# Performance work log

Measured on AMD Instinct MI355X. Metric: run time of the kernel, lower is better.

## Reference

```python
import jax, jax.numpy as jnp
import numpy as np

EPS_DENOM = 1e-7   # epsilon added to sigmoid-sum denominator in the torch code
EPS_NORM = 1e-5    # torch InstanceNorm1d default eps


def _fcnn(x, W1, b1, W2, b2):
    # FCNN: Linear -> ReLU -> Linear
    return jax.nn.relu(x @ W1 + b1) @ W2 + b2


def setup_inputs() -> dict:
    key = jax.random.key(0)
    N, E, D, H = 100000, 1600000, 32, 128  # nodes, edges, feature dim (c_in1=c_out2), hidden (c_out1)
    ks = jax.random.split(key, 11)
    node_features = jax.random.normal(ks[0], (N, D), jnp.float32)
    edge_features = jax.random.normal(ks[1], (E, D), jnp.float32)
    edge_index = jax.random.randint(ks[2], (2, E), 0, N, dtype=jnp.int64)
    sD = 1.0 / np.sqrt(D)
    sH = 1.0 / np.sqrt(H)
    # FCNN_one params
    W1a = jax.random.normal(ks[3], (D, H), jnp.float32) * sD
    b1a = jax.random.normal(ks[4], (H,), jnp.float32) * sD
    W2a = jax.random.normal(ks[5], (H, D), jnp.float32) * sH
    b2a = jax.random.normal(ks[6], (D,), jnp.float32) * sH
    # FCNN_two params
    W1b = jax.random.normal(ks[7], (D, H), jnp.float32) * sD
    b1b = jax.random.normal(ks[8], (H,), jnp.float32) * sD
    W2b = jax.random.normal(ks[9], (H, D), jnp.float32) * sH
    b2b = jax.random.normal(ks[10], (D,), jnp.float32) * sH
    return dict(node_features=node_features, edge_features=edge_features,
                W1a=W1a, b1a=b1a, W2a=W2a, b2a=b2a,
                W1b=W1b, b1b=b1b, W2b=W2b, b2b=b2b,
                edge_index=edge_index)


def reference(node_features, edge_features, W1a, b1a, W2a, b2a,
              W1b, b1b, W2b, b2b, edge_index):
    x = node_features                      # [N, D]
    N = x.shape[0]
    h1 = _fcnn(x, W1a, b1a, W2a, b2a)      # FCNN_one(x_i) for all nodes
    h2 = _fcnn(x, W1b, b1b, W2b, b2b)      # FCNN_two(x_j) for all nodes

    s = jax.nn.sigmoid(edge_features)      # [E, D]
    # node i gathers edges where it is src OR dst (both directions)
    seg = jnp.concatenate([edge_index[0], edge_index[1]])  # [2E] center node
    nbr = jnp.concatenate([edge_index[1], edge_index[0]])  # [2E] neighbor node
    s2 = jnp.concatenate([s, s], axis=0)                   # [2E, D]

    denom = EPS_DENOM + jax.ops.segment_sum(s2, seg, num_segments=N)  # [N, D]
    msg = (s2 / denom[seg]) * h2[nbr]                                 # [2E, D]
    agg = jax.ops.segment_sum(msg, seg, num_segments=N)               # [N, D]

    h = h1 + agg
    # InstanceNorm1d over the feature dim (no affine, biased variance); dropout is identity (eval)
    mu = jnp.mean(h, axis=-1, keepdims=True)
    var = jnp.var(h, axis=-1, keepdims=True)
    hn = (h - mu) * jax.lax.rsqrt(var + EPS_NORM)
    return x + jax.nn.relu(hn)
```

## Files before the change

### kernel.cpp

```cpp
#include <hip/hip_runtime.h>

#define EPS_DENOM 1e-7f
#define EPS_NORM  1e-5f

static constexpr int D  = 32;
static constexpr int H  = 128;
static constexpr int BK = 128;
static constexpr int CHUNK = 3072;
static constexpr int CAPMAX = 6144;

typedef _Float16 f16x8 __attribute__((ext_vector_type(8)));
typedef float    f32x4 __attribute__((ext_vector_type(4)));

__global__ __launch_bounds__(256) void fcnn_mfma_kernel(
    const float* __restrict__ x,
    const float* __restrict__ W1a, const float* __restrict__ b1a,
    const float* __restrict__ W2a, const float* __restrict__ b2a,
    const float* __restrict__ W1b, const float* __restrict__ b1b,
    const float* __restrict__ W2b, const float* __restrict__ b2b,
    float* __restrict__ h1, _Float16* __restrict__ h2h, int N)
{
    __shared__ _Float16 lds[30208];
    _Float16* xk = lds;

    const int tid = threadIdx.x;
    const int nb0 = blockIdx.x * 64;

    #pragma unroll
    for (int t = 0; t < 8; ++t) {
        int f = t * 256 + tid;
        int node = f >> 5, off = f & 31;
        int gn = nb0 + node;
        float v = (gn < N) ? x[(size_t)gn * 32 + off] : 0.0f;
        xk[node * 40 + off] = (_Float16)v;
    }
    for (int fc = 0; fc < 2; ++fc) {
        const float* W1 = fc ? W1b : W1a;
        const float* W2 = fc ? W2b : W2a;
        _Float16* w1t = lds + 2560 + fc * 5120;
        _Float16* w2t = lds + 12800 + fc * 4352;
        #pragma unroll
        for (int t = 0; t < 16; ++t) {
            int f = t * 256 + tid;
            w1t[(f & 127) * 40 + (f >> 7)] = (_Float16)W1[f];
        }
        #pragma unroll
        for (int t = 0; t < 16; ++t) {
            int f = t * 256 + tid;
            w2t[(f & 31) * 136 + (f >> 5)] = (_Float16)W2[f];
        }
    }
    __syncthreads();

    const int wid  = tid >> 6;
    const int lane = tid & 63;
    const int m    = lane & 15;
    const int g    = lane >> 4;
    _Float16* t1 = lds + 21504 + wid * 2176;

    f16x8 ax = *(const f16x8*)(xk + (wid * 16 + m) * 40 + g * 8);

    for (int fc = 0; fc < 2; ++fc) {
        const float* b1v = fc ? b1b : b1a;
        const float* b2v = fc ? b2b : b2a;
        const _Float16* w1t = lds + 2560 + fc * 5120;
        const _Float16* w2t = lds + 12800 + fc * 4352;

        for (int hb = 0; hb < 8; ++hb) {
            f16x8 bw = *(const f16x8*)(w1t + (hb * 16 + m) * 40 + g * 8);
            f32x4 c = {0.f, 0.f, 0.f, 0.f};
            c = __builtin_amdgcn_mfma_f32_16x16x32_f16(ax, bw, c, 0, 0, 0);
            float bias = b1v[hb * 16 + m];
            #pragma unroll
            for (int r = 0; r < 4; ++r) {
                float tv = fmaxf(c[r] + bias, 0.0f);
                t1[(g * 4 + r) * 136 + hb * 16 + m] = (_Float16)tv;
            }
        }

        for (int dt = 0; dt < 2; ++dt) {
            f32x4 c2 = {0.f, 0.f, 0.f, 0.f};
            #pragma unroll
            for (int kc = 0; kc < 4; ++kc) {
                f16x8 a2  = *(const f16x8*)(t1 + m * 136 + kc * 32 + g * 8);
                f16x8 b2w = *(const f16x8*)(w2t + (dt * 16 + m) * 136 + kc * 32 + g * 8);
                c2 = __builtin_amdgcn_mfma_f32_16x16x32_f16(a2, b2w, c2, 0, 0, 0);
            }
            float bias = b2v[dt * 16 + m];
            #pragma unroll
            for (int r = 0; r < 4; ++r) {
                int gn = nb0 + wid * 16 + g * 4 + r;
                if (gn < N) {
                    float val = c2[r] + bias;
                    if (fc == 0) h1[(size_t)gn * 32 + dt * 16 + m] = val;
                    else         h2h[(size_t)gn * 32 + dt * 16 + m] = (_Float16)val;
                }
            }
        }
        __syncthreads();
    }
}

__global__ __launch_bounds__(256) void sprep_kernel(
    const float* __restrict__ ef, _Float16* __restrict__ sgh, int n4)
{
    int i = blockIdx.x * blockDim.x + threadIdx.x;
    if (i >= n4) return;
    float4 v = ((const float4*)ef)[i];
    _Float16 r[4];
    r[0] = (_Float16)(1.0f / (1.0f + __expf(-v.x)));
    r[1] = (_Float16)(1.0f / (1.0f + __expf(-v.y)));
    r[2] = (_Float16)(1.0f / (1.0f + __expf(-v.z)));
    r[3] = (_Float16)(1.0f / (1.0f + __expf(-v.w)));
    ((uint2*)sgh)[i] = *(const uint2*)r;
}

__global__ __launch_bounds__(256) void bin1_kernel(
    const int* __restrict__ ei, int* __restrict__ gcursor,
    uint2* __restrict__ gadj, int E, int CAP)
{
    __shared__ uint2 recs[2 * CHUNK];
    __shared__ int cnt[1024];
    __shared__ int offs[1024];
    __shared__ int gbase[1024];
    __shared__ int partial[256];

    const int tid  = threadIdx.x;
    const int base = blockIdx.x * CHUNK;
    const int ne   = min(CHUNK, E - base);

    #pragma unroll
    for (int i = 0; i < 4; ++i) cnt[tid * 4 + i] = 0;
    __syncthreads();

    int av[CHUNK / 256], bv[CHUNK / 256];
    #pragma unroll
    for (int j = 0; j < CHUNK / 256; ++j) {
        int r = j * 256 + tid;
        if (r < ne) {
            int e = base + r;
            av[j] = ei[e]; bv[j] = ei[E + e];
            atomicAdd(&cnt[av[j] >> 7], 1);
            atomicAdd(&cnt[bv[j] >> 7], 1);
        } else av[j] = -1;
    }
    __syncthreads();

    int c0 = cnt[tid*4], c1 = cnt[tid*4+1], c2 = cnt[tid*4+2], c3 = cnt[tid*4+3];
    int psum = c0 + c1 + c2 + c3;
    partial[tid] = psum;
    __syncthreads();
    for (int off = 1; off < 256; off <<= 1) {
        int t = (tid >= off) ? partial[tid - off] : 0;
        __syncthreads();
        partial[tid] += t;
        __syncthreads();
    }
    int ex = partial[tid] - psum;
    offs[tid*4]   = ex;
    offs[tid*4+1] = ex + c0;
    offs[tid*4+2] = ex + c0 + c1;
    offs[tid*4+3] = ex + c0 + c1 + c2;
    cnt[tid*4]    = ex;
    cnt[tid*4+1]  = ex + c0;
    cnt[tid*4+2]  = ex + c0 + c1;
    cnt[tid*4+3]  = ex + c0 + c1 + c2;
    __syncthreads();

    #pragma unroll
    for (int j = 0; j < CHUNK / 256; ++j) {
        if (av[j] >= 0) {
            int e = base + j * 256 + tid;
            int a = av[j], b = bv[j];
            int pa = atomicAdd(&cnt[a >> 7], 1);
            recs[pa] = make_uint2(((unsigned)(a & 127) << 21) | (unsigned)e,
                                  ((unsigned)(a >> 7) << 17) | (unsigned)b);
            int pb = atomicAdd(&cnt[b >> 7], 1);
            recs[pb] = make_uint2(((unsigned)(b & 127) << 21) | (unsigned)e,
                                  ((unsigned)(b >> 7) << 17) | (unsigned)a);
        }
    }
    __syncthreads();

    #pragma unroll
    for (int i = 0; i < 4; ++i) {
        int bidx = tid * 4 + i;
        int c = cnt[bidx] - offs[bidx];
        if (c > 0) gbase[bidx] = atomicAdd(&gcursor[bidx], c);
    }
    __syncthreads();

    int total = 2 * ne;
    for (int i = tid; i < total; i += 256) {
        uint2 r = recs[i];
        int bidx = r.y >> 17;
        int dest = gbase[bidx] + (i - offs[bidx]);
        if (dest < CAP)
            gadj[(size_t)bidx * CAP + dest] = r;
    }
}

__global__ __launch_bounds__(256) void bin2_kernel(
    const int* __restrict__ gcursor, uint2* __restrict__ gadj,
    int* __restrict__ gstart, int* __restrict__ gdeg,
    int N, int CAP)
{
    __shared__ uint2 recs[CAPMAX];
    __shared__ int cnt[BK];
    __shared__ int sc[BK];
    __shared__ int lcur[BK];

    const int tid = threadIdx.x;
    const int bk  = blockIdx.x;
    const int count = min(gcursor[bk], CAP);
    uint2* seg = gadj + (size_t)bk * CAP;

    if (tid < BK) cnt[tid] = 0;
    for (int i = tid; i < count; i += 256) recs[i] = seg[i];
    __syncthreads();

    for (int i = tid; i < count; i += 256)
        atomicAdd(&cnt[(recs[i].x >> 21) & 127], 1);
    __syncthreads();

    int v = (tid < BK) ? cnt[tid] : 0;
    if (tid < BK) sc[tid] = v;
    __syncthreads();
    for (int off = 1; off < BK; off <<= 1) {
        int t = (tid < BK && tid >= off) ? sc[tid - off] : 0;
        __syncthreads();
        if (tid < BK) sc[tid] += t;
        __syncthreads();
    }
    if (tid < BK) {
        int excl = sc[tid] - v;
        lcur[tid] = excl;
        int gn = bk * BK + tid;
        if (gn < N) {
            gstart[gn] = bk * CAP + excl;
            gdeg[gn]   = v;
        }
    }
    __syncthreads();

    for (int i = tid; i < count; i += 256) {
        uint2 r = recs[i];
        int l = (r.x >> 21) & 127;
        int pos = atomicAdd(&lcur[l], 1);
        seg[pos] = make_uint2(r.x & 0x1FFFFFu, r.y & 0x1FFFFu);
    }
}

template <bool USE_SG>
__global__ __launch_bounds__(256) void gather_kernel(
    const float* __restrict__ x,  const _Float16* __restrict__ sgh,
    const float* __restrict__ ef, const float* __restrict__ h1,
    const _Float16* __restrict__ h2h,
    const int* __restrict__ gstart, const int* __restrict__ gdeg,
    const uint2* __restrict__ adj2,
    float* __restrict__ out, int N)
{
    int t = blockIdx.x * blockDim.x + threadIdx.x;
    int n = t >> 5;
    int d = t & 31;
    if (n >= N) return;

    int start = gstart[n];
    int end   = start + gdeg[n];

    float s_sum = 0.0f, sh_sum = 0.0f;
    int k = start;
    for (; k + 4 <= end; k += 4) {
        uint2 r0 = adj2[k+0], r1 = adj2[k+1], r2 = adj2[k+2], r3 = adj2[k+3];
        float s0, s1, s2, s3;
        if (USE_SG) {
            s0 = (float)sgh[(size_t)r0.x * 32 + d];
            s1 = (float)sgh[(size_t)r1.x * 32 + d];
            s2 = (float)sgh[(size_t)r2.x * 32 + d];
            s3 = (float)sgh[(size_t)r3.x * 32 + d];
        } else {
            s0 = 1.0f / (1.0f + __expf(-ef[(size_t)r0.x * 32 + d]));
            s1 = 1.0f / (1.0f + __expf(-ef[(size_t)r1.x * 32 + d]));
            s2 = 1.0f / (1.0f + __expf(-ef[(size_t)r2.x * 32 + d]));
            s3 = 1.0f / (1.0f + __expf(-ef[(size_t)r3.x * 32 + d]));
        }
        float h0 = (float)h2h[(size_t)r0.y * 32 + d];
        float h1v = (float)h2h[(size_t)r1.y * 32 + d];
        float h2v = (float)h2h[(size_t)r2.y * 32 + d];
        float h3 = (float)h2h[(size_t)r3.y * 32 + d];
        s_sum += (s0 + s1) + (s2 + s3);
        sh_sum = fmaf(s0, h0, sh_sum);
        sh_sum = fmaf(s1, h1v, sh_sum);
        sh_sum = fmaf(s2, h2v, sh_sum);
        sh_sum = fmaf(s3, h3, sh_sum);
    }
    for (; k < end; ++k) {
        uint2 r = adj2[k];
        float s;
        if (USE_SG) s = (float)sgh[(size_t)r.x * 32 + d];
        else        s = 1.0f / (1.0f + __expf(-ef[(size_t)r.x * 32 + d]));
        float hh = (float)h2h[(size_t)r.y * 32 + d];
        s_sum += s;
        sh_sum = fmaf(s, hh, sh_sum);
    }

    size_t idx = (size_t)n * 32 + d;
    float h = h1[idx] + sh_sum / (EPS_DENOM + s_sum);

    float sum = h, sq = h * h;
    #pragma unroll
    for (int off = 16; off > 0; off >>= 1) {
        sum += __shfl_xor(sum, off, 32);
        sq  += __shfl_xor(sq,  off, 32);
    }
    float mu  = sum * (1.0f / 32.0f);
    float var = fmaxf(sq * (1.0f / 32.0f) - mu * mu, 0.0f);
    float hn  = (h - mu) * rsqrtf(var + EPS_NORM);

    out[idx] = x[idx] + fmaxf(hn, 0.0f);
}

extern "C" void kernel_launch(void* const* d_in, const int* in_sizes, int n_in,
                              void* d_out, int out_size, void* d_ws, size_t ws_size,
                              hipStream_t stream)
{
    const float* x   = (const float*)d_in[0];
    const float* ef  = (const float*)d_in[1];
    const float* W1a = (const float*)d_in[2];
    const float* b1a = (const float*)d_in[3];
    const float* W2a = (const float*)d_in[4];
    const float* b2a = (const float*)d_in[5];
    const float* W1b = (const float*)d_in[6];
    const float* b1b = (const float*)d_in[7];
    const float* W2b = (const float*)d_in[8];
    const float* b2b = (const float*)d_in[9];
    const int*   ei  = (const int*)d_in[10];
    float* out = (float*)d_out;

    const int N  = in_sizes[0] / D;
    const int E  = in_sizes[1] / D;
    const int NB = (N + BK - 1) / BK;
    int CAP = (2 * E) / NB;
    CAP = CAP + CAP / 2;
    CAP = (CAP + 255) & ~255;
    if (CAP > CAPMAX) CAP = CAPMAX;

    char* p = (char*)d_ws;
    float*    h1      = (float*)p;    p += (size_t)N * 32 * 4;
    _Float16* h2h     = (_Float16*)p; p += (size_t)N * 32 * 2;
    int*      gcursor = (int*)p;      p += 1024 * 4;
    int*      gstart  = (int*)p;      p += (size_t)N * 4;
    int*      gdeg    = (int*)p;      p += (size_t)N * 4;
    uint2*    gadj    = (uint2*)p;    p += (size_t)NB * CAP * 8;
    _Float16* sgh     = (_Float16*)p;
    const bool use_sg = ((size_t)(p - (char*)d_ws) + (size_t)E * 64) <= ws_size;

    hipMemsetAsync(gcursor, 0, 1024 * 4, stream);

    fcnn_mfma_kernel<<<(N + 63) / 64, 256, 0, stream>>>(
        x, W1a, b1a, W2a, b2a, W1b, b1b, W2b, b2b, h1, h2h, N);

    if (use_sg) {
        int n4 = E * 8;
        sprep_kernel<<<(n4 + 255) / 256, 256, 0, stream>>>(ef, sgh, n4);
    }

    bin1_kernel<<<(E + CHUNK - 1) / CHUNK, 256, 0, stream>>>(ei, gcursor, gadj, E, CAP);
    bin2_kernel<<<NB, 256, 0, stream>>>(gcursor, gadj, gstart, gdeg, N, CAP);

    int gthreads = N * 32;
    if (use_sg)
        gather_kernel<true><<<(gthreads + 255) / 256, 256, 0, stream>>>(
            x, sgh, ef, h1, h2h, gstart, gdeg, gadj, out, N);
    else
        gather_kernel<false><<<(gthreads + 255) / 256, 256, 0, stream>>>(
            x, sgh, ef, h1, h2h, gstart, gdeg, gadj, out, N);
}
```

Before: 558.4 us.

## Fuse sigmoid into binning and scatter 8-bit quantized payloads per adjacency slot

Removes the separate sigmoid-precompute kernel. The binning kernel now computes the sigmoid of each edge's features, quantizes them to 8 bits in LDS, and writes a 32-byte payload alongside each adjacency record into per-bucket storage. The gather kernel then reads these payloads from bucket-local memory rather than from scattered fp16 rows. This cuts the bytes per edge gather and improves locality. In exchange the sigmoid has only 8-bit precision (error up to about 0.002), which may hurt accuracy, and the binning chunk shrinks to fit the extra LDS, which adds more blocks and more global atomics.

```diff
diff --git a/kernel.cpp b/kernel.cpp
--- a/kernel.cpp
+++ b/kernel.cpp
@@ -6,7 +6,7 @@
 static constexpr int D  = 32;
 static constexpr int H  = 128;
 static constexpr int BK = 128;
-static constexpr int CHUNK = 3072;
+static constexpr int CHUNK = 1024;
 static constexpr int CAPMAX = 6144;
 
 typedef _Float16 f16x8 __attribute__((ext_vector_type(8)));
@@ -101,25 +101,13 @@
     }
 }
 
-__global__ __launch_bounds__(256) void sprep_kernel(
-    const float* __restrict__ ef, _Float16* __restrict__ sgh, int n4)
-{
-    int i = blockIdx.x * blockDim.x + threadIdx.x;
-    if (i >= n4) return;
-    float4 v = ((const float4*)ef)[i];
-    _Float16 r[4];
-    r[0] = (_Float16)(1.0f / (1.0f + __expf(-v.x)));
-    r[1] = (_Float16)(1.0f / (1.0f + __expf(-v.y)));
-    r[2] = (_Float16)(1.0f / (1.0f + __expf(-v.z)));
-    r[3] = (_Float16)(1.0f / (1.0f + __expf(-v.w)));
-    ((uint2*)sgh)[i] = *(const uint2*)r;
-}
-
 __global__ __launch_bounds__(256) void bin1_kernel(
-    const int* __restrict__ ei, int* __restrict__ gcursor,
-    uint2* __restrict__ gadj, int E, int CAP)
+    const int* __restrict__ ei, const float* __restrict__ ef,
+    int* __restrict__ gcursor, uint2* __restrict__ gadj,
+    unsigned char* __restrict__ pay, int E, int CAP, int paymode)
 {
     __shared__ uint2 recs[2 * CHUNK];
+    __shared__ uint4 srows4[CHUNK * 2];
     __shared__ int cnt[1024];
     __shared__ int offs[1024];
     __shared__ int gbase[1024];
@@ -143,6 +131,25 @@
             atomicAdd(&cnt[av[j] >> 7], 1);
             atomicAdd(&cnt[bv[j] >> 7], 1);
         } else av[j] = -1;
+    }
+
+    if (paymode) {
+        const float4* efc = (const float4*)(ef + (size_t)base * 32);
+        uchar4* sc4 = (uchar4*)srows4;
+        const int nf4 = ne * 8;
+        #pragma unroll
+        for (int j = 0; j < CHUNK * 8 / 256; ++j) {
+            int fidx = j * 256 + tid;
+            if (fidx < nf4) {
+                float4 v = efc[fidx];
+                uchar4 q;
+                q.x = (unsigned char)(255.0f / (1.0f + __expf(-v.x)) + 0.5f);
+                q.y = (unsigned char)(255.0f / (1.0f + __expf(-v.y)) + 0.5f);
+                q.z = (unsigned char)(255.0f / (1.0f + __expf(-v.z)) + 0.5f);
+                q.w = (unsigned char)(255.0f / (1.0f + __expf(-v.w)) + 0.5f);
+                sc4[fidx] = q;
+            }
+        }
     }
     __syncthreads();
 
@@ -190,20 +197,30 @@
     }
     __syncthreads();
 
+    const unsigned char* srows = (const unsigned char*)srows4;
     int total = 2 * ne;
     for (int i = tid; i < total; i += 256) {
         uint2 r = recs[i];
         int bidx = r.y >> 17;
         int dest = gbase[bidx] + (i - offs[bidx]);
-        if (dest < CAP)
-            gadj[(size_t)bidx * CAP + dest] = r;
+        if (dest < CAP) {
+            size_t slot = (size_t)bidx * CAP + dest;
+            gadj[slot] = r;
+            if (paymode) {
+                int le = (int)(r.x & 0x1FFFFFu) - base;
+                const uint4* sr = (const uint4*)(srows + le * 32);
+                uint4 s0 = sr[0], s1 = sr[1];
+                uint4* pd = (uint4*)(pay + slot * 32);
+                pd[0] = s0; pd[1] = s1;
+            }
+        }
     }
 }
 
 __global__ __launch_bounds__(256) void bin2_kernel(
     const int* __restrict__ gcursor, uint2* __restrict__ gadj,
     int* __restrict__ gstart, int* __restrict__ gdeg,
-    int N, int CAP)
+    int N, int CAP, int paymode)
 {
     __shared__ uint2 recs[CAPMAX];
     __shared__ int cnt[BK];
@@ -247,18 +264,19 @@
         uint2 r = recs[i];
         int l = (r.x >> 21) & 127;
         int pos = atomicAdd(&lcur[l], 1);
-        seg[pos] = make_uint2(r.x & 0x1FFFFFu, r.y & 0x1FFFFu);
-    }
-}
-
-template <bool USE_SG>
+        unsigned xv = paymode ? (unsigned)i : (r.x & 0x1FFFFFu);
+        seg[pos] = make_uint2(xv, r.y & 0x1FFFFu);
+    }
+}
+
+template <int MODE>
 __global__ __launch_bounds__(256) void gather_kernel(
-    const float* __restrict__ x,  const _Float16* __restrict__ sgh,
-    const float* __restrict__ ef, const float* __restrict__ h1,
-    const _Float16* __restrict__ h2h,
+    const float* __restrict__ x,  const float* __restrict__ ef,
+    const unsigned char* __restrict__ pay,
+    const float* __restrict__ h1, const _Float16* __restrict__ h2h,
     const int* __restrict__ gstart, const int* __restrict__ gdeg,
     const uint2* __restrict__ adj2,
-    float* __restrict__ out, int N)
+    float* __restrict__ out, int N, int CAP)
 {
     int t = blockIdx.x * blockDim.x + threadIdx.x;
     int n = t >> 5;
@@ -267,17 +285,18 @@
 
     int start = gstart[n];
     int end   = start + gdeg[n];
+    const unsigned char* payb = pay + (size_t)(n >> 7) * CAP * 32 + d;
 
     float s_sum = 0.0f, sh_sum = 0.0f;
     int k = start;
     for (; k + 4 <= end; k += 4) {
         uint2 r0 = adj2[k+0], r1 = adj2[k+1], r2 = adj2[k+2], r3 = adj2[k+3];
         float s0, s1, s2, s3;
-        if (USE_SG) {
-            s0 = (float)sgh[(size_t)r0.x * 32 + d];
-            s1 = (float)sgh[(size_t)r1.x * 32 + d];
-            s2 = (float)sgh[(size_t)r2.x * 32 + d];
-            s3 = (float)sgh[(size_t)r3.x * 32 + d];
+        if (MODE) {
+            s0 = (float)payb[(size_t)r0.x * 32] * (1.0f / 255.0f);
+            s1 = (float)payb[(size_t)r1.x * 32] * (1.0f / 255.0f);
+            s2 = (float)payb[(size_t)r2.x * 32] * (1.0f / 255.0f);
+            s3 = (float)payb[(size_t)r3.x * 32] * (1.0f / 255.0f);
         } else {
             s0 = 1.0f / (1.0f + __expf(-ef[(size_t)r0.x * 32 + d]));
             s1 = 1.0f / (1.0f + __expf(-ef[(size_t)r1.x * 32 + d]));
@@ -297,8 +316,8 @@
     for (; k < end; ++k) {
         uint2 r = adj2[k];
         float s;
-        if (USE_SG) s = (float)sgh[(size_t)r.x * 32 + d];
-        else        s = 1.0f / (1.0f + __expf(-ef[(size_t)r.x * 32 + d]));
+        if (MODE) s = (float)payb[(size_t)r.x * 32] * (1.0f / 255.0f);
+        else      s = 1.0f / (1.0f + __expf(-ef[(size_t)r.x * 32 + d]));
         float hh = (float)h2h[(size_t)r.y * 32 + d];
         s_sum += s;
         sh_sum = fmaf(s, hh, sh_sum);
@@ -351,28 +370,28 @@
     int*      gcursor = (int*)p;      p += 1024 * 4;
     int*      gstart  = (int*)p;      p += (size_t)N * 4;
     int*      gdeg    = (int*)p;      p += (size_t)N * 4;
+    p = (char*)(((uintptr_t)p + 31) & ~(uintptr_t)31);
     uint2*    gadj    = (uint2*)p;    p += (size_t)NB * CAP * 8;
-    _Float16* sgh     = (_Float16*)p;
-    const bool use_sg = ((size_t)(p - (char*)d_ws) + (size_t)E * 64) <= ws_size;
+    p = (char*)(((uintptr_t)p + 31) & ~(uintptr_t)31);
+    unsigned char* pay = (unsigned char*)p;
+    const bool use_pay =
+        ((size_t)(p - (char*)d_ws) + (size_t)NB * CAP * 32) <= ws_size;
+    const int paymode = use_pay ? 1 : 0;
 
     hipMemsetAsync(gcursor, 0, 1024 * 4, stream);
 
     fcnn_mfma_kernel<<<(N + 63) / 64, 256, 0, stream>>>(
         x, W1a, b1a, W2a, b2a, W1b, b1b, W2b, b2b, h1, h2h, N);
 
-    if (use_sg) {
-        int n4 = E * 8;
-        sprep_kernel<<<(n4 + 255) / 256, 256, 0, stream>>>(ef, sgh, n4);
-    }
-
-    bin1_kernel<<<(E + CHUNK - 1) / CHUNK, 256, 0, stream>>>(ei, gcursor, gadj, E, CAP);
-    bin2_kernel<<<NB, 256, 0, stream>>>(gcursor, gadj, gstart, gdeg, N, CAP);
+    bin1_kernel<<<(E + CHUNK - 1) / CHUNK, 256, 0, stream>>>(
+        ei, ef, gcursor, gadj, pay, E, CAP, paymode);
+    bin2_kernel<<<NB, 256, 0, stream>>>(gcursor, gadj, gstart, gdeg, N, CAP, paymode);
 
     int gthreads = N * 32;
-    if (use_sg)
-        gather_kernel<true><<<(gthreads + 255) / 256, 256, 0, stream>>>(
-            x, sgh, ef, h1, h2h, gstart, gdeg, gadj, out, N);
+    if (use_pay)
+        gather_kernel<1><<<(gthreads + 255) / 256, 256, 0, stream>>>(
+            x, ef, pay, h1, h2h, gstart, gdeg, gadj, out, N, CAP);
     else
-        gather_kernel<false><<<(gthreads + 255) / 256, 256, 0, stream>>>(
-            x, sgh, ef, h1, h2h, gstart, gdeg, gadj, out, N);
-}
+        gather_kernel<0><<<(gthreads + 255) / 256, 256, 0, stream>>>(
+            x, ef, pay, h1, h2h, gstart, gdeg, gadj, out, N, CAP);
+}
```

Result: slower. 652.3 us (+16.8%).

## Fuse local sort and gather into per-bucket LDS-atomic aggregation kernel

Applied to the files above, without the earlier changes.

Replaces the second binning pass (per-node counting sort within each bucket) and the per-node gather kernel with one kernel per 128-node bucket. That kernel accumulates sigmoid and sigmoid*h2 sums into shared-memory arrays with atomics, then applies instance norm and writes the output. It also drops the fp16 sigmoid precompute pass and computes the sigmoid from the fp32 edge features inline. This removes a kernel launch, the gstart/gdeg arrays and a global rewrite of the adjacency, at the cost of LDS atomic contention and reading fp32 edge features instead of fp16.

```diff
diff --git a/kernel.cpp b/kernel.cpp
--- a/kernel.cpp
+++ b/kernel.cpp
@@ -7,7 +7,6 @@
 static constexpr int H  = 128;
 static constexpr int BK = 128;
 static constexpr int CHUNK = 3072;
-static constexpr int CAPMAX = 6144;
 
 typedef _Float16 f16x8 __attribute__((ext_vector_type(8)));
 typedef float    f32x4 __attribute__((ext_vector_type(4)));
@@ -101,20 +100,6 @@
     }
 }
 
-__global__ __launch_bounds__(256) void sprep_kernel(
-    const float* __restrict__ ef, _Float16* __restrict__ sgh, int n4)
-{
-    int i = blockIdx.x * blockDim.x + threadIdx.x;
-    if (i >= n4) return;
-    float4 v = ((const float4*)ef)[i];
-    _Float16 r[4];
-    r[0] = (_Float16)(1.0f / (1.0f + __expf(-v.x)));
-    r[1] = (_Float16)(1.0f / (1.0f + __expf(-v.y)));
-    r[2] = (_Float16)(1.0f / (1.0f + __expf(-v.z)));
-    r[3] = (_Float16)(1.0f / (1.0f + __expf(-v.w)));
-    ((uint2*)sgh)[i] = *(const uint2*)r;
-}
-
 __global__ __launch_bounds__(256) void bin1_kernel(
     const int* __restrict__ ei, int* __restrict__ gcursor,
     uint2* __restrict__ gadj, int E, int CAP)
@@ -200,124 +185,79 @@
     }
 }
 
-__global__ __launch_bounds__(256) void bin2_kernel(
-    const int* __restrict__ gcursor, uint2* __restrict__ gadj,
-    int* __restrict__ gstart, int* __restrict__ gdeg,
-    int N, int CAP)
+__global__ __launch_bounds__(512) void agg_kernel(
+    const int* __restrict__ gcursor, const uint2* __restrict__ gadj,
+    const float* __restrict__ ef, const float* __restrict__ x,
+    const float* __restrict__ h1, const _Float16* __restrict__ h2h,
+    float* __restrict__ out, int N, int CAP)
 {
-    __shared__ uint2 recs[CAPMAX];
-    __shared__ int cnt[BK];
-    __shared__ int sc[BK];
-    __shared__ int lcur[BK];
+    __shared__ float acc_s [BK * 32];
+    __shared__ float acc_sh[BK * 32];
 
     const int tid = threadIdx.x;
     const int bk  = blockIdx.x;
     const int count = min(gcursor[bk], CAP);
-    uint2* seg = gadj + (size_t)bk * CAP;
-
-    if (tid < BK) cnt[tid] = 0;
-    for (int i = tid; i < count; i += 256) recs[i] = seg[i];
-    __syncthreads();
-
-    for (int i = tid; i < count; i += 256)
-        atomicAdd(&cnt[(recs[i].x >> 21) & 127], 1);
-    __syncthreads();
-
-    int v = (tid < BK) ? cnt[tid] : 0;
-    if (tid < BK) sc[tid] = v;
-    __syncthreads();
-    for (int off = 1; off < BK; off <<= 1) {
-        int t = (tid < BK && tid >= off) ? sc[tid - off] : 0;
-        __syncthreads();
-        if (tid < BK) sc[tid] += t;
-        __syncthreads();
-    }
-    if (tid < BK) {
-        int excl = sc[tid] - v;
-        lcur[tid] = excl;
-        int gn = bk * BK + tid;
-        if (gn < N) {
-            gstart[gn] = bk * CAP + excl;
-            gdeg[gn]   = v;
-        }
-    }
-    __syncthreads();
-
-    for (int i = tid; i < count; i += 256) {
-        uint2 r = recs[i];
+    const uint2* seg = gadj + (size_t)bk * CAP;
+
+    for (int i = tid; i < BK * 32; i += 512) {
+        acc_s[i]  = 0.0f;
+        acc_sh[i] = 0.0f;
+    }
+    __syncthreads();
+
+    const int g = tid >> 5;
+    const int d = tid & 31;
+
+    int k = g;
+    for (; k + 16 < count; k += 32) {
+        uint2 r0 = seg[k];
+        uint2 r1 = seg[k + 16];
+        int e0 = r0.x & 0x1FFFFF, e1 = r1.x & 0x1FFFFF;
+        float v0 = ef[(size_t)e0 * 32 + d];
+        float v1 = ef[(size_t)e1 * 32 + d];
+        float hv0 = (float)h2h[(size_t)(r0.y & 0x1FFFF) * 32 + d];
+        float hv1 = (float)h2h[(size_t)(r1.y & 0x1FFFF) * 32 + d];
+        float s0 = 1.0f / (1.0f + __expf(-v0));
+        float s1 = 1.0f / (1.0f + __expf(-v1));
+        int l0 = (r0.x >> 21) & 127;
+        int l1 = (r1.x >> 21) & 127;
+        atomicAdd(&acc_s [l0 * 32 + d], s0);
+        atomicAdd(&acc_sh[l0 * 32 + d], s0 * hv0);
+        atomicAdd(&acc_s [l1 * 32 + d], s1);
+        atomicAdd(&acc_sh[l1 * 32 + d], s1 * hv1);
+    }
+    if (k < count) {
+        uint2 r = seg[k];
+        int e = r.x & 0x1FFFFF;
+        float v = ef[(size_t)e * 32 + d];
+        float hv = (float)h2h[(size_t)(r.y & 0x1FFFF) * 32 + d];
+        float s = 1.0f / (1.0f + __expf(-v));
         int l = (r.x >> 21) & 127;
-        int pos = atomicAdd(&lcur[l], 1);
-        seg[pos] = make_uint2(r.x & 0x1FFFFFu, r.y & 0x1FFFFu);
-    }
-}
-
-template <bool USE_SG>
-__global__ __launch_bounds__(256) void gather_kernel(
-    const float* __restrict__ x,  const _Float16* __restrict__ sgh,
-    const float* __restrict__ ef, const float* __restrict__ h1,
-    const _Float16* __restrict__ h2h,
-    const int* __restrict__ gstart, const int* __restrict__ gdeg,
-    const uint2* __restrict__ adj2,
-    float* __restrict__ out, int N)
-{
-    int t = blockIdx.x * blockDim.x + threadIdx.x;
-    int n = t >> 5;
-    int d = t & 31;
-    if (n >= N) return;
-
-    int start = gstart[n];
-    int end   = start + gdeg[n];
-
-    float s_sum = 0.0f, sh_sum = 0.0f;
-    int k = start;
-    for (; k + 4 <= end; k += 4) {
-        uint2 r0 = adj2[k+0], r1 = adj2[k+1], r2 = adj2[k+2], r3 = adj2[k+3];
-        float s0, s1, s2, s3;
-        if (USE_SG) {
-            s0 = (float)sgh[(size_t)r0.x * 32 + d];
-            s1 = (float)sgh[(size_t)r1.x * 32 + d];
-            s2 = (float)sgh[(size_t)r2.x * 32 + d];
-            s3 = (float)sgh[(size_t)r3.x * 32 + d];
-        } else {
-            s0 = 1.0f / (1.0f + __expf(-ef[(size_t)r0.x * 32 + d]));
-            s1 = 1.0f / (1.0f + __expf(-ef[(size_t)r1.x * 32 + d]));
-            s2 = 1.0f / (1.0f + __expf(-ef[(size_t)r2.x * 32 + d]));
-            s3 = 1.0f / (1.0f + __expf(-ef[(size_t)r3.x * 32 + d]));
-        }
-        float h0 = (float)h2h[(size_t)r0.y * 32 + d];
-        float h1v = (float)h2h[(size_t)r1.y * 32 + d];
-        float h2v = (float)h2h[(size_t)r2.y * 32 + d];
-        float h3 = (float)h2h[(size_t)r3.y * 32 + d];
-        s_sum += (s0 + s1) + (s2 + s3);
-        sh_sum = fmaf(s0, h0, sh_sum);
-        sh_sum = fmaf(s1, h1v, sh_sum);
-        sh_sum = fmaf(s2, h2v, sh_sum);
-        sh_sum = fmaf(s3, h3, sh_sum);
-    }
-    for (; k < end; ++k) {
-        uint2 r = adj2[k];
-        float s;
-        if (USE_SG) s = (float)sgh[(size_t)r.x * 32 + d];
-        else        s = 1.0f / (1.0f + __expf(-ef[(size_t)r.x * 32 + d]));
-        float hh = (float)h2h[(size_t)r.y * 32 + d];
-        s_sum += s;
-        sh_sum = fmaf(s, hh, sh_sum);
-    }
-
-    size_t idx = (size_t)n * 32 + d;
-    float h = h1[idx] + sh_sum / (EPS_DENOM + s_sum);
-
-    float sum = h, sq = h * h;
-    #pragma unroll
-    for (int off = 16; off > 0; off >>= 1) {
-        sum += __shfl_xor(sum, off, 32);
-        sq  += __shfl_xor(sq,  off, 32);
-    }
-    float mu  = sum * (1.0f / 32.0f);
-    float var = fmaxf(sq * (1.0f / 32.0f) - mu * mu, 0.0f);
-    float hn  = (h - mu) * rsqrtf(var + EPS_NORM);
-
-    out[idx] = x[idx] + fmaxf(hn, 0.0f);
+        atomicAdd(&acc_s [l * 32 + d], s);
+        atomicAdd(&acc_sh[l * 32 + d], s * hv);
+    }
+    __syncthreads();
+
+    for (int li = g; li < BK; li += 16) {
+        int gn = bk * BK + li;
+        if (gn >= N) break;
+        size_t idx = (size_t)gn * 32 + d;
+        float ssum = acc_s [li * 32 + d];
+        float shs  = acc_sh[li * 32 + d];
+        float h = h1[idx] + shs / (EPS_DENOM + ssum);
+
+        float sum = h, sq = h * h;
+        #pragma unroll
+        for (int off = 16; off > 0; off >>= 1) {
+            sum += __shfl_xor(sum, off, 32);
+            sq  += __shfl_xor(sq,  off, 32);
+        }
+        float mu  = sum * (1.0f / 32.0f);
+        float var = fmaxf(sq * (1.0f / 32.0f) - mu * mu, 0.0f);
+        float hn  = (h - mu) * rsqrtf(var + EPS_NORM);
+
+        out[idx] = x[idx] + fmaxf(hn, 0.0f);
+    }
 }
 
 extern "C" void kernel_launch(void* const* d_in, const int* in_sizes, int n_in,
@@ -343,36 +283,21 @@
     int CAP = (2 * E) / NB;
     CAP = CAP + CAP / 2;
     CAP = (CAP + 255) & ~255;
-    if (CAP > CAPMAX) CAP = CAPMAX;
 
     char* p = (char*)d_ws;
     float*    h1      = (float*)p;    p += (size_t)N * 32 * 4;
     _Float16* h2h     = (_Float16*)p; p += (size_t)N * 32 * 2;
     int*      gcursor = (int*)p;      p += 1024 * 4;
-    int*      gstart  = (int*)p;      p += (size_t)N * 4;
-    int*      gdeg    = (int*)p;      p += (size_t)N * 4;
+    p = (char*)(((uintptr_t)p + 31) & ~(uintptr_t)31);
     uint2*    gadj    = (uint2*)p;    p += (size_t)NB * CAP * 8;
-    _Float16* sgh     = (_Float16*)p;
-    const bool use_sg = ((size_t)(p - (char*)d_ws) + (size_t)E * 64) <= ws_size;
+    (void)ws_size;
 
     hipMemsetAsync(gcursor, 0, 1024 * 4, stream);
 
     fcnn_mfma_kernel<<<(N + 63) / 64, 256, 0, stream>>>(
         x, W1a, b1a, W2a, b2a, W1b, b1b, W2b, b2b, h1, h2h, N);
 
-    if (use_sg) {
-        int n4 = E * 8;
-        sprep_kernel<<<(n4 + 255) / 256, 256, 0, stream>>>(ef, sgh, n4);
-    }
-
     bin1_kernel<<<(E + CHUNK - 1) / CHUNK, 256, 0, stream>>>(ei, gcursor, gadj, E, CAP);
-    bin2_kernel<<<NB, 256, 0, stream>>>(gcursor, gadj, gstart, gdeg, N, CAP);
-
-    int gthreads = N * 32;
-    if (use_sg)
-        gather_kernel<true><<<(gthreads + 255) / 256, 256, 0, stream>>>(
-            x, sgh, ef, h1, h2h, gstart, gdeg, gadj, out, N);
-    else
-        gather_kernel<false><<<(gthreads + 255) / 256, 256, 0, stream>>>(
-            x, sgh, ef, h1, h2h, gstart, gdeg, gadj, out, N);
+
+    agg_kernel<<<NB, 512, 0, stream>>>(gcursor, gadj, ef, x, h1, h2h, out, N, CAP);
 }
```

After: 1.695 ms. +203.5%, slower.
